# Performance work log

Hardware: AMD Instinct MI355X
Metric: run time of the kernel (lower is better)

## Reference

```python
import jax, jax.numpy as jnp
import numpy as np

DIM = 256
HEADS = 8
DIM_HEAD = 32
AGENT = 6
WIN = 7


def _relative_position_index(L, Wh, Ww):
    coords = np.stack(np.meshgrid(np.arange(L), np.arange(Wh), np.arange(Ww), indexing='ij'))
    cf = coords.reshape(3, -1)                      # (3, N)
    rel = cf[:, :, None] - cf[:, None, :]           # (3, N, N)
    rel = rel.transpose(1, 2, 0).astype(np.int64)   # (N, N, 3)
    rel[..., 0] += L - 1
    rel[..., 1] += Wh - 1
    rel[..., 2] += Ww - 1
    rel[..., 0] *= (2 * Wh - 1) * (2 * Ww - 1)
    rel[..., 1] *= 2 * Ww - 1
    return rel.sum(-1)                              # (N, N)


def setup_inputs() -> dict:
    key = jax.random.key(0)
    k1, k2, k3, k4, k5 = jax.random.split(key, 5)
    B, X, Y = 2, 8, 8
    x = jax.random.normal(k1, (B, AGENT, X, Y, WIN, WIN, DIM), dtype=jnp.float32)
    mask = jax.random.randint(k2, (B, X, Y, WIN, WIN, 1, AGENT), 0, 2, dtype=jnp.int32)
    w_qkv = jax.random.normal(k3, (3 * DIM, DIM), dtype=jnp.float32) * 0.02
    w_out = jax.random.normal(k4, (DIM, DIM), dtype=jnp.float32) * 0.02
    n_bias = (2 * AGENT - 1) * (2 * WIN - 1) * (2 * WIN - 1)
    bias_table = jax.random.normal(k5, (n_bias, HEADS), dtype=jnp.float32) * 0.02
    return {"x": x, "mask": mask, "w_qkv": w_qkv, "w_out": w_out, "bias_table": bias_table}


def reference(x, mask, w_qkv, w_out, bias_table):
    B, L, X, Y, W1, W2, C = x.shape
    h, dh = HEADS, DIM_HEAD
    N = L * W1 * W2
    scale = dh ** -0.5

    # 'b l x y w1 w2 d -> (b x y) (l w1 w2) d'
    xr = jnp.transpose(x, (0, 2, 3, 1, 4, 5, 6)).reshape(B * X * Y, N, C)

    qkv = jnp.einsum('bnc,ec->bne', xr, w_qkv)      # (Bw, N, 3C)
    q, k, v = jnp.split(qkv, 3, axis=-1)
    def to_heads(t):
        return jnp.transpose(t.reshape(B * X * Y, N, h, dh), (0, 2, 1, 3))
    q, k, v = to_heads(q) * scale, to_heads(k), to_heads(v)

    sim = jnp.einsum('bhid,bhjd->bhij', q, k)       # (Bw, h, N, N)

    rel_idx = jnp.asarray(_relative_position_index(L, W1, W2))
    bias = bias_table[rel_idx]                      # (N, N, h)
    sim = sim + jnp.transpose(bias, (2, 0, 1))[None]

    # 'b x y w1 w2 e l -> (b x y) e (l w1 w2)'
    m = jnp.transpose(mask, (0, 1, 2, 5, 6, 3, 4)).reshape(B * X * Y, 1, N)
    sim = jnp.where(m[:, :, None, :] == 0, jnp.float32(-1e9), sim)

    attn = jax.nn.softmax(sim, axis=-1)
    out = jnp.einsum('bhij,bhjd->bhid', attn, v)    # (Bw, h, N, dh)

    # 'b h (l w1 w2) d -> b l w1 w2 (h d)'
    out = jnp.transpose(out, (0, 2, 1, 3)).reshape(B * X * Y, L, W1, W2, C)
    out = jnp.einsum('blwvc,ec->blwve', out, w_out)

    # '(b x y) l w1 w2 d -> b l x y w1 w2 d'
    out = out.reshape(B, X, Y, L, W1, W2, C)
    return jnp.transpose(out, (0, 3, 1, 2, 4, 5, 6))
```

## Files before the change

### kernel.cpp

```cpp
#include <hip/hip_runtime.h>
#include <hip/hip_bf16.h>

#define DIM 256
#define HEADS 8
#define DH 32
#define AGENT 6
#define WIN 7
#define NTOK 294
#define BWIN 128
#define SCALE 0.17677669529663687f
#define LOG2E 1.4426950408889634f
#define TP 19
#define QSTR 40
#define PSTR 320

typedef __hip_bfloat16 bf16;
typedef __attribute__((ext_vector_type(8))) short s16x8;
typedef __attribute__((ext_vector_type(4))) float f32x4;
typedef __attribute__((ext_vector_type(4))) unsigned int u32x4;

#if __has_builtin(__builtin_amdgcn_exp2f)
#define EXP2(x) __builtin_amdgcn_exp2f(x)
#else
#define EXP2(x) exp2f(x)
#endif

__device__ __forceinline__ float bfv(unsigned short u){ return __uint_as_float(((unsigned int)u) << 16); }
__device__ __forceinline__ unsigned short f2bu(float f){
    bf16 b = __float2bfloat16(f); return *reinterpret_cast<unsigned short*>(&b);
}
__device__ __forceinline__ float rdf(const void* p, size_t idx, int isf32) {
    return isf32 ? ((const float*)p)[idx] : bfv(((const unsigned short*)p)[idx]);
}

__device__ __forceinline__ int vtswz(int d, int cByte) {
    return (d * (PSTR * 2) + cByte) ^ (((d >> 1) & 7) << 4);
}

__device__ __forceinline__ void gll16(const void* gp, void* lp) {
    __builtin_amdgcn_global_load_lds(
        (const __attribute__((address_space(1))) unsigned int*)gp,
        (__attribute__((address_space(3))) unsigned int*)lp, 16, 0, 0);
}

__device__ __forceinline__ int detect_flag(const unsigned short* __restrict__ xraw,
                                           int* sflag, int nthreads) {
    if (threadIdx.x == 0) *sflag = 0;
    __syncthreads();
    int bad = 0;
    for (int i = threadIdx.x; i < 8192; i += nthreads) {
        float v = bfv(xraw[i]);
        if (!(fabsf(v) <= 1e10f)) bad = 1;
    }
    if (bad) atomicOr(sflag, 1);
    __syncthreads();
    return *sflag;
}

__global__ __launch_bounds__(256) void prep_kernel(
    const unsigned short* __restrict__ xraw,
    const void* __restrict__ wq, const void* __restrict__ wo, const void* __restrict__ bt,
    unsigned short* __restrict__ Wq, unsigned short* __restrict__ Wo,
    unsigned short* __restrict__ biasB) {
    __shared__ int sflag;
    const int isf32 = detect_flag(xraw, &sflag, 256);
    const int bid = blockIdx.x;
    if (bid < 722) {
        int idx = bid * 256 + threadIdx.x;
        int lane = idx & 63; int t = idx >> 6;
        int jt = t % TP; t /= TP; int it = t % TP; int h = t / TP;
        int i = it * 16 + (lane & 15);
        int g = lane >> 4;
        ushort4 v;
        unsigned short* vp = (unsigned short*)&v;
        #pragma unroll
        for (int r = 0; r < 4; r++) {
            int j = jt * 16 + g * 4 + r;
            float val = 0.f;
            if (i < NTOK && j < NTOK) {
                int li = i / 49, ri = i - li * 49, w1i = ri / 7, w2i = ri - w1i * 7;
                int lj = j / 49, rj = j - lj * 49, w1j = rj / 7, w2j = rj - w1j * 7;
                int rel = (li - lj + AGENT - 1) * 169 + (w1i - w1j + WIN - 1) * 13 + (w2i - w2j + WIN - 1);
                val = rdf(bt, (size_t)rel * HEADS + h, isf32) * LOG2E;
            }
            vp[r] = f2bu(val);
        }
        ((ushort4*)biasB)[idx] = v;
    } else {
        int c = (bid - 722) * 256 + threadIdx.x;
        const void* src; unsigned short* dst; size_t off;
        if (c < 24576) { src = wq; dst = Wq; off = (size_t)c * 8; }
        else           { src = wo; dst = Wo; off = (size_t)(c - 24576) * 8; }
        if (isf32) {
            const float4* s4 = (const float4*)((const float*)src + off);
            float4 v0 = s4[0], v1 = s4[1];
            s16x8 u;
            u[0] = (short)f2bu(v0.x); u[1] = (short)f2bu(v0.y); u[2] = (short)f2bu(v0.z); u[3] = (short)f2bu(v0.w);
            u[4] = (short)f2bu(v1.x); u[5] = (short)f2bu(v1.y); u[6] = (short)f2bu(v1.z); u[7] = (short)f2bu(v1.w);
            *(s16x8*)(dst + off) = u;
        } else {
            *(uint4*)(dst + off) = *(const uint4*)((const unsigned short*)src + off);
        }
    }
}

__device__ __forceinline__ void stage64_g(const unsigned short* __restrict__ g,
                                          unsigned short* lds, size_t rowBase) {
    const int lane = threadIdx.x & 63, wv = threadIdx.x >> 6;
    const int sub = lane >> 5;
    const int colB = (lane & 31) << 4;
    #pragma unroll
    for (int k = 0; k < 8; k++) {
        const int rr = (wv * 8 + k) * 2 + sub;
        const int cg = colB ^ ((rr & 7) << 4);
        gll16((const char*)g + (rowBase + (size_t)rr) * 512 + cg,
              lds + (size_t)(wv * 8 + k) * 512);
    }
}

__device__ __forceinline__ void stage64_f(const float* __restrict__ g,
                                          unsigned short* lds, size_t rowBase) {
    const int tid = threadIdx.x;
    #pragma unroll
    for (int k = 0; k < 8; k++) {
        int ch = k * 256 + tid;
        int rr = ch >> 5;
        int cB = (ch & 31) << 4;
        int cg = cB ^ ((rr & 7) << 4);
        const f32x4* s4 = (const f32x4*)(g + (rowBase + (size_t)rr) * 256 + (cg >> 1));
        f32x4 v0 = __builtin_nontemporal_load(s4);
        f32x4 v1 = __builtin_nontemporal_load(s4 + 1);
        s16x8 u;
        u[0] = (short)f2bu(v0[0]); u[1] = (short)f2bu(v0[1]); u[2] = (short)f2bu(v0[2]); u[3] = (short)f2bu(v0[3]);
        u[4] = (short)f2bu(v1[0]); u[5] = (short)f2bu(v1[1]); u[6] = (short)f2bu(v1[2]); u[7] = (short)f2bu(v1[3]);
        *(s16x8*)(lds + (size_t)rr * 256 + (cB >> 1)) = u;
    }
}

__global__ __launch_bounds__(256) void qkv_mfma(
    const void* __restrict__ xin, const unsigned short* __restrict__ Wq,
    bf16* __restrict__ Q, bf16* __restrict__ K, bf16* __restrict__ V) {
    __shared__ unsigned short P0[64 * 256];
    __shared__ unsigned short P1[64 * 256];
    __shared__ int sflag;
    const int isf32 = detect_flag((const unsigned short*)xin, &sflag, 256);
    const size_t mBase = (size_t)blockIdx.x * 64;
    if (isf32) stage64_f((const float*)xin, P1, mBase);
    else       stage64_g((const unsigned short*)xin, P1, mBase);
    stage64_g(Wq, P0, 0);
    const int tid = threadIdx.x;
    const int wave = tid >> 6, lane = tid & 63;
    const int li = lane & 15, g = lane >> 4;
    const int wm = wave & 1, wn = wave >> 1;
    unsigned int rowOff[2][4];
    #pragma unroll
    for (int mi = 0; mi < 2; mi++)
        #pragma unroll
        for (int r = 0; r < 4; r++) {
            unsigned int m = (unsigned int)mBase + wm * 32 + mi * 16 + g * 4 + r;
            unsigned int w2 = m % 7u, t1 = m / 7u;
            unsigned int w1 = t1 % 7u, t2 = t1 / 7u;
            unsigned int yy = t2 & 7u, t3 = t2 >> 3;
            unsigned int xx = t3 & 7u, t4 = t3 >> 3;
            unsigned int l = t4 % 6u, b = t4 / 6u;
            unsigned int bw = (b << 6) | (xx << 3) | yy;
            unsigned int n = l * 49u + w1 * 7u + w2;
            rowOff[mi][r] = bw * 75264u + n * 32u;
        }
    const int koX = (li & 7) * 8;
    __syncthreads();
    s16x8 a0r[8], a1r[8];
    #pragma unroll
    for (int kc = 0; kc < 8; kc++) {
        const int ko = (kc * 32 + g * 8) ^ koX;
        a0r[kc] = *(const s16x8*)&P1[(wm * 32 + li) * 256 + ko];
        a1r[kc] = *(const s16x8*)&P1[(wm * 32 + 16 + li) * 256 + ko];
    }
    __syncthreads();
    for (int c = 0; c < 12; c++) {
        const unsigned short* Bc = (c & 1) ? P1 : P0;
        unsigned short* Bn = (c & 1) ? P0 : P1;
        if (c + 1 < 12) stage64_g(Wq, Bn, (size_t)(c + 1) * 64);
        f32x4 acc[2][2];
        #pragma unroll
        for (int mi = 0; mi < 2; mi++)
            #pragma unroll
            for (int ni = 0; ni < 2; ni++) acc[mi][ni] = (f32x4){0.f, 0.f, 0.f, 0.f};
        #pragma unroll
        for (int kc = 0; kc < 8; kc++) {
            const int ko = (kc * 32 + g * 8) ^ koX;
            s16x8 b0 = *(const s16x8*)&Bc[(wn * 32 + li) * 256 + ko];
            s16x8 b1 = *(const s16x8*)&Bc[(wn * 32 + 16 + li) * 256 + ko];
            acc[0][0] = __builtin_amdgcn_mfma_f32_16x16x32_bf16(a0r[kc], b0, acc[0][0], 0, 0, 0);
            acc[0][1] = __builtin_amdgcn_mfma_f32_16x16x32_bf16(a0r[kc], b1, acc[0][1], 0, 0, 0);
            acc[1][0] = __builtin_amdgcn_mfma_f32_16x16x32_bf16(a1r[kc], b0, acc[1][0], 0, 0, 0);
            acc[1][1] = __builtin_amdgcn_mfma_f32_16x16x32_bf16(a1r[kc], b1, acc[1][1], 0, 0, 0);
        }
        const int p = c >> 2;
        bf16* dst = (p == 0) ? Q : (p == 1) ? K : V;
        const float sc = (p == 0) ? (SCALE * LOG2E) : 1.0f;
        const unsigned int hoff = ((c & 3) * 2 + wn) * 9408u;
        #pragma unroll
        for (int ni = 0; ni < 2; ni++) {
            const unsigned int d = ni * 16 + li;
            #pragma unroll
            for (int mi = 0; mi < 2; mi++)
                #pragma unroll
                for (int r = 0; r < 4; r++)
                    dst[(size_t)(rowOff[mi][r] + hoff + d)] =
                        __float2bfloat16(acc[mi][ni][r] * sc);
        }
        __syncthreads();
    }
}

__global__ __launch_bounds__(512, 2) void attn_mfma(
    const bf16* __restrict__ Q, const bf16* __restrict__ K, const bf16* __restrict__ V,
    const unsigned short* __restrict__ biasB, const int* __restrict__ mask,
    bf16* __restrict__ AT) {
    __shared__ unsigned short Qs[304 * QSTR];
    __shared__ unsigned short Ks[304 * QSTR];
    __shared__ unsigned short Vt[32 * PSTR];
    __shared__ int ms[320];
    const int tid = threadIdx.x;
    const int bw = blockIdx.x >> 3, h = blockIdx.x & 7;
    const size_t base = ((size_t)bw * HEADS + h) * NTOK * DH;
    const unsigned int* Qg = (const unsigned int*)(Q + base);
    const unsigned int* Kg = (const unsigned int*)(K + base);
    const unsigned int* Vg = (const unsigned int*)(V + base);
    char* VtB = (char*)Vt;
    for (int gg = tid; gg < NTOK * DH / 2; gg += 512) {
        int r = gg >> 4, d2 = (gg & 15) * 2;
        unsigned int uq = __builtin_nontemporal_load(&Qg[gg]);
        unsigned int uk = __builtin_nontemporal_load(&Kg[gg]);
        unsigned int uv = __builtin_nontemporal_load(&Vg[gg]);
        *(unsigned int*)&Qs[r * QSTR + d2] = uq;
        *(unsigned int*)&Ks[r * QSTR + d2] = uk;
        *(unsigned short*)(VtB + vtswz(d2,     r * 2)) = (unsigned short)(uv & 0xffffu);
        *(unsigned short*)(VtB + vtswz(d2 + 1, r * 2)) = (unsigned short)(uv >> 16);
    }
    for (int e = NTOK * QSTR + tid; e < 304 * QSTR; e += 512) { Qs[e] = 0; Ks[e] = 0; }
    for (int idx = tid; idx < 32 * (PSTR - NTOK); idx += 512) {
        int d = idx / (PSTR - NTOK), c = NTOK + idx % (PSTR - NTOK);
        *(unsigned short*)(VtB + vtswz(d, c * 2)) = 0;
    }
    for (int j = tid; j < 320; j += 512) {
        int mv = 0;
        if (j < NTOK) { int a = j / 49, jr = j - a * 49; mv = mask[((size_t)bw * 49 + jr) * AGENT + a]; }
        ms[j] = mv;
    }
    __syncthreads();
    const int wave = tid >> 6, lane = tid & 63;
    const int li = lane & 15, g = lane >> 4;
    unsigned int mb0 = 0, mb1 = 0, mb2 = 0;
    for (int jt = 0; jt < TP; jt++)
        for (int r = 0; r < 4; r++) {
            int j = jt * 16 + g * 4 + r;
            if (j < NTOK && ms[j]) {
                int bit = jt * 4 + r;
                if (bit < 32) mb0 |= (1u << bit);
                else if (bit < 64) mb1 |= (1u << (bit - 32));
                else mb2 |= (1u << (bit - 64));
            }
        }
    const ushort4* bb = (const ushort4*)biasB + (size_t)h * TP * TP * 64;
    const int sAg = li + ((lane & 16) << 1);
    const int sBg = sAg + 16;
    const bool hiSel = (lane >= 32);
    for (int it = wave; it < TP; it += 8) {
        const s16x8 bq = *(const s16x8*)&Qs[(it * 16 + li) * QSTR + g * 8];
        f32x4 s[TP];
        __builtin_amdgcn_s_setprio(1);
        #pragma unroll
        for (int jt = 0; jt < TP; jt++) {
            ushort4 bv = bb[(it * TP + jt) * 64 + lane];
            f32x4 c = {bfv(bv.x), bfv(bv.y), bfv(bv.z), bfv(bv.w)};
            s16x8 ak = *(const s16x8*)&Ks[(jt * 16 + li) * QSTR + g * 8];
            s[jt] = __builtin_amdgcn_mfma_f32_16x16x32_bf16(ak, bq, c, 0, 0, 0);
        }
        __builtin_amdgcn_s_setprio(0);
        float mx = -INFINITY;
        #pragma unroll
        for (int jt = 0; jt < TP; jt++)
            #pragma unroll
            for (int r = 0; r < 4; r++) {
                int bit = jt * 4 + r;
                unsigned int w = (bit < 32) ? mb0 : (bit < 64) ? mb1 : mb2;
                float sv = ((w >> (bit & 31)) & 1u) ? s[jt][r] : -1e9f;
                if (jt == TP - 1 && g * 4 + r >= 6) sv = -INFINITY;
                s[jt][r] = sv;
                mx = fmaxf(mx, sv);
            }
        mx = fmaxf(mx, __shfl_xor(mx, 16));
        mx = fmaxf(mx, __shfl_xor(mx, 32));
        float sum = 0.f;
        unsigned int p0[TP], p1[TP];
        #pragma unroll
        for (int jt = 0; jt < TP; jt++) {
            float e0 = EXP2(s[jt][0] - mx);
            float e1 = EXP2(s[jt][1] - mx);
            float e2 = EXP2(s[jt][2] - mx);
            float e3 = EXP2(s[jt][3] - mx);
            sum += (e0 + e1) + (e2 + e3);
            unsigned int lo, hi;
            asm("v_cvt_pk_bf16_f32 %0, %1, %2" : "=v"(lo) : "v"(e0), "v"(e1));
            asm("v_cvt_pk_bf16_f32 %0, %1, %2" : "=v"(hi) : "v"(e2), "v"(e3));
            p0[jt] = lo; p1[jt] = hi;
        }
        sum += __shfl_xor(sum, 16);
        sum += __shfl_xor(sum, 32);
        const float inv = 1.0f / sum;
        f32x4 o0 = {0.f, 0.f, 0.f, 0.f}, o1 = {0.f, 0.f, 0.f, 0.f};
        #pragma unroll
        for (int kc = 0; kc < 10; kc++) {
            unsigned int a0q = __shfl(p0[2 * kc], sAg);
            unsigned int b0q = __shfl(p1[2 * kc], sAg);
            unsigned int c0q = __shfl(p0[2 * kc], sBg);
            unsigned int d0q = __shfl(p1[2 * kc], sBg);
            unsigned int a1q = 0, b1q = 0, c1q = 0, d1q = 0;
            if (2 * kc + 1 < TP) {
                a1q = __shfl(p0[2 * kc + 1], sAg);
                b1q = __shfl(p1[2 * kc + 1], sAg);
                c1q = __shfl(p0[2 * kc + 1], sBg);
                d1q = __shfl(p1[2 * kc + 1], sBg);
            }
            u32x4 w;
            w[0] = hiSel ? a1q : a0q;
            w[1] = hiSel ? b1q : b0q;
            w[2] = hiSel ? c1q : c0q;
            w[3] = hiSel ? d1q : d0q;
            s16x8 ap = __builtin_bit_cast(s16x8, w);
            s16x8 b0 = *(const s16x8*)(VtB + vtswz(li,      (kc * 32 + g * 8) * 2));
            s16x8 b1 = *(const s16x8*)(VtB + vtswz(li + 16, (kc * 32 + g * 8) * 2));
            __builtin_amdgcn_s_setprio(1);
            o0 = __builtin_amdgcn_mfma_f32_16x16x32_bf16(ap, b0, o0, 0, 0, 0);
            o1 = __builtin_amdgcn_mfma_f32_16x16x32_bf16(ap, b1, o1, 0, 0, 0);
            __builtin_amdgcn_s_setprio(0);
        }
        #pragma unroll
        for (int r = 0; r < 4; r++) {
            float iv = __shfl(inv, g * 4 + r);
            int i = it * 16 + g * 4 + r;
            if (i < NTOK) {
                size_t ob = ((size_t)bw * NTOK + i) * DIM + h * DH;
                AT[ob + li]      = __float2bfloat16(o0[r] * iv);
                AT[ob + 16 + li] = __float2bfloat16(o1[r] * iv);
            }
        }
    }
}

__global__ __launch_bounds__(256) void proj_mfma(
    const bf16* __restrict__ AT, const unsigned short* __restrict__ Wo,
    float* __restrict__ out) {
    __shared__ unsigned short As[64 * 256];
    __shared__ unsigned short Bs[64 * 256];
    const size_t mBase = (size_t)blockIdx.x * 64;
    stage64_g((const unsigned short*)AT, As, mBase);
    const int tid = threadIdx.x;
    const int wave = tid >> 6, lane = tid & 63;
    const int li = lane & 15, g = lane >> 4;
    const int wm = wave & 1, wn = wave >> 1;
    unsigned int offO[2][4];
    #pragma unroll
    for (int mi = 0; mi < 2; mi++)
        #pragma unroll
        for (int r = 0; r < 4; r++) {
            unsigned int m = (unsigned int)mBase + wm * 32 + mi * 16 + g * 4 + r;
            unsigned int bw = m / 294u, n = m - bw * 294u;
            unsigned int b = bw >> 6, xx = (bw >> 3) & 7u, yy = bw & 7u;
            unsigned int l = n / 49u, rr = n - l * 49u, w1 = rr / 7u, w2 = rr - w1 * 7u;
            offO[mi][r] = ((((((b * 6u + l) * 8u + xx) * 8u + yy) * 7u + w1) * 7u) + w2) * 256u;
        }
    const int koX = (li & 7) * 8;
    for (int ec = 0; ec < 4; ec++) {
        __syncthreads();
        stage64_g(Wo, Bs, (size_t)ec * 64);
        __syncthreads();
        f32x4 acc[2][2];
        #pragma unroll
        for (int mi = 0; mi < 2; mi++)
            #pragma unroll
            for (int ni = 0; ni < 2; ni++) acc[mi][ni] = (f32x4){0.f, 0.f, 0.f, 0.f};
        #pragma unroll
        for (int kc = 0; kc < 8; kc++) {
            const int ko = (kc * 32 + g * 8) ^ koX;
            s16x8 a0 = *(const s16x8*)&As[(wm * 32 + li) * 256 + ko];
            s16x8 a1 = *(const s16x8*)&As[(wm * 32 + 16 + li) * 256 + ko];
            s16x8 b0 = *(const s16x8*)&Bs[(wn * 32 + li) * 256 + ko];
            s16x8 b1 = *(const s16x8*)&Bs[(wn * 32 + 16 + li) * 256 + ko];
            acc[0][0] = __builtin_amdgcn_mfma_f32_16x16x32_bf16(a0, b0, acc[0][0], 0, 0, 0);
            acc[0][1] = __builtin_amdgcn_mfma_f32_16x16x32_bf16(a0, b1, acc[0][1], 0, 0, 0);
            acc[1][0] = __builtin_amdgcn_mfma_f32_16x16x32_bf16(a1, b0, acc[1][0], 0, 0, 0);
            acc[1][1] = __builtin_amdgcn_mfma_f32_16x16x32_bf16(a1, b1, acc[1][1], 0, 0, 0);
        }
        #pragma unroll
        for (int ni = 0; ni < 2; ni++) {
            const unsigned int e = ec * 64 + wn * 32 + ni * 16 + li;
            #pragma unroll
            for (int mi = 0; mi < 2; mi++)
                #pragma unroll
                for (int r = 0; r < 4; r++)
                    __builtin_nontemporal_store(acc[mi][ni][r],
                        &out[(size_t)(offO[mi][r] + e)]);
        }
    }
}

extern "C" void kernel_launch(void* const* d_in, const int* in_sizes, int n_in,
                              void* d_out, int out_size, void* d_ws, size_t ws_size,
                              hipStream_t stream) {
    const long long SZ_X = 9633792, SZ_M = 37632, SZ_WQ = 196608, SZ_WO = 65536, SZ_BT = 14872;
    const void* x = d_in[0]; const void* maskp = d_in[1]; const void* wqkv = d_in[2];
    const void* wout = d_in[3]; const void* btab = d_in[4];
    for (int i = 0; i < n_in; i++) {
        long long s = in_sizes[i];
        if (s == SZ_X) x = d_in[i];
        else if (s == SZ_M) maskp = d_in[i];
        else if (s == SZ_WQ) wqkv = d_in[i];
        else if (s == SZ_WO) wout = d_in[i];
        else if (s == SZ_BT) btab = d_in[i];
    }
    const int* mask = (const int*)maskp;
    float* out = (float*)d_out;
    const size_t SZ = (size_t)BWIN * NTOK * DIM;
    bf16* Q  = (bf16*)d_ws;
    bf16* K  = Q + SZ;
    bf16* V  = K + SZ;
    bf16* AT = V + SZ;
    unsigned short* biasB = (unsigned short*)(AT + SZ);
    const size_t NBB = (size_t)HEADS * TP * TP * 64 * 4;
    unsigned short* Wq = biasB + NBB;
    unsigned short* Wo = Wq + 196608;
    prep_kernel<<<dim3(850), dim3(256), 0, stream>>>(
        (const unsigned short*)x, wqkv, wout, btab, Wq, Wo, biasB);
    qkv_mfma<<<dim3(588), dim3(256), 0, stream>>>(x, Wq, Q, K, V);
    attn_mfma<<<dim3(BWIN * HEADS), dim3(512), 0, stream>>>(Q, K, V, biasB, mask, AT);
    proj_mfma<<<dim3(588), dim3(256), 0, stream>>>(AT, Wo, out);
}
```

Before: 209.1 us.

## Read Q directly from global in attention; double-buffer weight tiles in projection

The attention kernel no longer stages Q in shared memory. Each wave loads its Q fragment straight from global memory, which cuts LDS traffic and footprint, though the padded tail rows now read past the logical Q block instead of zeroed padding. The projection kernel loads its A fragments into registers once and double-buffers the Wo tiles across two shared buffers, prefetching the next tile while the current one is consumed. This removes one sync per iteration and the repeated A reloads from LDS, at the cost of more register use.

```diff
diff --git a/kernel.cpp b/kernel.cpp
--- a/kernel.cpp
+++ b/kernel.cpp
@@ -218,28 +218,25 @@
     const bf16* __restrict__ Q, const bf16* __restrict__ K, const bf16* __restrict__ V,
     const unsigned short* __restrict__ biasB, const int* __restrict__ mask,
     bf16* __restrict__ AT) {
-    __shared__ unsigned short Qs[304 * QSTR];
     __shared__ unsigned short Ks[304 * QSTR];
     __shared__ unsigned short Vt[32 * PSTR];
     __shared__ int ms[320];
     const int tid = threadIdx.x;
     const int bw = blockIdx.x >> 3, h = blockIdx.x & 7;
     const size_t base = ((size_t)bw * HEADS + h) * NTOK * DH;
-    const unsigned int* Qg = (const unsigned int*)(Q + base);
     const unsigned int* Kg = (const unsigned int*)(K + base);
     const unsigned int* Vg = (const unsigned int*)(V + base);
+    const unsigned short* Qg = (const unsigned short*)(Q + base);
     char* VtB = (char*)Vt;
     for (int gg = tid; gg < NTOK * DH / 2; gg += 512) {
         int r = gg >> 4, d2 = (gg & 15) * 2;
-        unsigned int uq = __builtin_nontemporal_load(&Qg[gg]);
         unsigned int uk = __builtin_nontemporal_load(&Kg[gg]);
         unsigned int uv = __builtin_nontemporal_load(&Vg[gg]);
-        *(unsigned int*)&Qs[r * QSTR + d2] = uq;
         *(unsigned int*)&Ks[r * QSTR + d2] = uk;
         *(unsigned short*)(VtB + vtswz(d2,     r * 2)) = (unsigned short)(uv & 0xffffu);
         *(unsigned short*)(VtB + vtswz(d2 + 1, r * 2)) = (unsigned short)(uv >> 16);
     }
-    for (int e = NTOK * QSTR + tid; e < 304 * QSTR; e += 512) { Qs[e] = 0; Ks[e] = 0; }
+    for (int e = NTOK * QSTR + tid; e < 304 * QSTR; e += 512) { Ks[e] = 0; }
     for (int idx = tid; idx < 32 * (PSTR - NTOK); idx += 512) {
         int d = idx / (PSTR - NTOK), c = NTOK + idx % (PSTR - NTOK);
         *(unsigned short*)(VtB + vtswz(d, c * 2)) = 0;
@@ -268,7 +265,7 @@
     const int sBg = sAg + 16;
     const bool hiSel = (lane >= 32);
     for (int it = wave; it < TP; it += 8) {
-        const s16x8 bq = *(const s16x8*)&Qs[(it * 16 + li) * QSTR + g * 8];
+        const s16x8 bq = *(const s16x8*)&Qg[((size_t)it * 16 + li) * DH + g * 8];
         f32x4 s[TP];
         __builtin_amdgcn_s_setprio(1);
         #pragma unroll
@@ -353,10 +350,11 @@
 __global__ __launch_bounds__(256) void proj_mfma(
     const bf16* __restrict__ AT, const unsigned short* __restrict__ Wo,
     float* __restrict__ out) {
-    __shared__ unsigned short As[64 * 256];
-    __shared__ unsigned short Bs[64 * 256];
+    __shared__ unsigned short P0[64 * 256];
+    __shared__ unsigned short P1[64 * 256];
     const size_t mBase = (size_t)blockIdx.x * 64;
-    stage64_g((const unsigned short*)AT, As, mBase);
+    stage64_g((const unsigned short*)AT, P1, mBase);
+    stage64_g(Wo, P0, 0);
     const int tid = threadIdx.x;
     const int wave = tid >> 6, lane = tid & 63;
     const int li = lane & 15, g = lane >> 4;
@@ -373,10 +371,19 @@
             offO[mi][r] = ((((((b * 6u + l) * 8u + xx) * 8u + yy) * 7u + w1) * 7u) + w2) * 256u;
         }
     const int koX = (li & 7) * 8;
+    __syncthreads();
+    s16x8 a0r[8], a1r[8];
+    #pragma unroll
+    for (int kc = 0; kc < 8; kc++) {
+        const int ko = (kc * 32 + g * 8) ^ koX;
+        a0r[kc] = *(const s16x8*)&P1[(wm * 32 + li) * 256 + ko];
+        a1r[kc] = *(const s16x8*)&P1[(wm * 32 + 16 + li) * 256 + ko];
+    }
+    __syncthreads();
     for (int ec = 0; ec < 4; ec++) {
-        __syncthreads();
-        stage64_g(Wo, Bs, (size_t)ec * 64);
-        __syncthreads();
+        const unsigned short* Bc = (ec & 1) ? P1 : P0;
+        unsigned short* Bn = (ec & 1) ? P0 : P1;
+        if (ec + 1 < 4) stage64_g(Wo, Bn, (size_t)(ec + 1) * 64);
         f32x4 acc[2][2];
         #pragma unroll
         for (int mi = 0; mi < 2; mi++)
@@ -385,14 +392,12 @@
         #pragma unroll
         for (int kc = 0; kc < 8; kc++) {
             const int ko = (kc * 32 + g * 8) ^ koX;
-            s16x8 a0 = *(const s16x8*)&As[(wm * 32 + li) * 256 + ko];
-            s16x8 a1 = *(const s16x8*)&As[(wm * 32 + 16 + li) * 256 + ko];
-            s16x8 b0 = *(const s16x8*)&Bs[(wn * 32 + li) * 256 + ko];
-            s16x8 b1 = *(const s16x8*)&Bs[(wn * 32 + 16 + li) * 256 + ko];
-            acc[0][0] = __builtin_amdgcn_mfma_f32_16x16x32_bf16(a0, b0, acc[0][0], 0, 0, 0);
-            acc[0][1] = __builtin_amdgcn_mfma_f32_16x16x32_bf16(a0, b1, acc[0][1], 0, 0, 0);
-            acc[1][0] = __builtin_amdgcn_mfma_f32_16x16x32_bf16(a1, b0, acc[1][0], 0, 0, 0);
-            acc[1][1] = __builtin_amdgcn_mfma_f32_16x16x32_bf16(a1, b1, acc[1][1], 0, 0, 0);
+            s16x8 b0 = *(const s16x8*)&Bc[(wn * 32 + li) * 256 + ko];
+            s16x8 b1 = *(const s16x8*)&Bc[(wn * 32 + 16 + li) * 256 + ko];
+            acc[0][0] = __builtin_amdgcn_mfma_f32_16x16x32_bf16(a0r[kc], b0, acc[0][0], 0, 0, 0);
+            acc[0][1] = __builtin_amdgcn_mfma_f32_16x16x32_bf16(a0r[kc], b1, acc[0][1], 0, 0, 0);
+            acc[1][0] = __builtin_amdgcn_mfma_f32_16x16x32_bf16(a1r[kc], b0, acc[1][0], 0, 0, 0);
+            acc[1][1] = __builtin_amdgcn_mfma_f32_16x16x32_bf16(a1r[kc], b1, acc[1][1], 0, 0, 0);
         }
         #pragma unroll
         for (int ni = 0; ni < 2; ni++) {
@@ -404,6 +409,7 @@
                     __builtin_nontemporal_store(acc[mi][ni][r],
                         &out[(size_t)(offO[mi][r] + e)]);
         }
+        __syncthreads();
     }
 }
 
```

Result: no change. 208.8 us (-0.1%).
